# Kernel optimization log

Measured on AMD Instinct MI355X. Metric: run time of the kernel, lower is better.

The kernel has to match this reference:

```python
import jax, jax.numpy as jnp
import numpy as np

B, LQ, LK, D, H = 8, 512, 512, 512, 128

def setup_inputs() -> dict:
    key = jax.random.key(0)
    k1, k2, k3, k4, k5 = jax.random.split(key, 5)
    qs = jax.random.normal(k1, (B, LQ, D), dtype=jnp.float32)
    ks = jax.random.normal(k2, (B, LK, D), dtype=jnp.float32)
    # Dense kernels: flax Dense stores kernel as [in_features, out_features]
    Wq = jax.random.normal(k3, (D, H), dtype=jnp.float32) / np.sqrt(D)
    Wk = jax.random.normal(k4, (D, H), dtype=jnp.float32) / np.sqrt(D)
    wv = jax.random.normal(k5, (H,), dtype=jnp.float32) / np.sqrt(H)
    return {"qs": qs, "ks": ks, "Wq": Wq, "Wk": Wk, "wv": wv}

def reference(qs, ks, Wq, Wk, wv):
    # Project queries and keys into the shared hidden space: [B,Lq,H], [B,Lk,H]
    q = jnp.einsum("bqd,dh->bqh", qs, Wq)
    k = jnp.einsum("bkd,dh->bkh", ks, Wk)
    # Broadcast-add -> tanh -> linear reduce over H: scores [B,Lq,Lk]
    feats = jnp.tanh(q[:, :, None, :] + k[:, None, :, :])  # [B,Lq,Lk,H]
    return jnp.einsum("bqkh,h->bqk", feats, wv)
```

## Files before the change

### kernel.cpp

```cpp
#include <hip/hip_runtime.h>
#include <hip/hip_bf16.h>
#include <cstdint>

#define B_   8
#define LQ_  512
#define LK_  512
#define D_   512
#define H_   128

typedef __attribute__((ext_vector_type(8))) short  short8;
typedef __attribute__((ext_vector_type(4))) float  float4v;

#define TANH_C 2.8853900817779268f

__device__ __forceinline__ short bf16rne(float x) {
  uint32_t u = __float_as_uint(x);
  return (short)((u + 0x7fffu + ((u >> 16) & 1u)) >> 16);
}

__global__ __launch_bounds__(256) void prep_kernel(
    const float* __restrict__ Wq, const float* __restrict__ Wk,
    const float* __restrict__ wv,
    short* __restrict__ WqF, short* __restrict__ WkF,
    float* __restrict__ w2, float* __restrict__ W0buf) {
  int g = blockIdx.x * 256 + threadIdx.x;
  if (blockIdx.x == 0) {
    int t = threadIdx.x;
    if (t < H_) w2[t] = -2.0f * wv[t];
    if (t == H_) {
      float s = 0.f;
      for (int h = 0; h < H_; ++h) s += wv[h];
      W0buf[0] = s;
    }
  }
  int m = g >> 13;
  int r = g & 8191;
  int l  = r & 63;
  int kb = (r >> 6) & 15;
  int nt = r >> 10;
  int col = nt * 16 + (l & 15);
  int k0  = kb * 32 + ((l >> 4) << 3);
  const float* W = m ? Wk : Wq;
  short8 f;
#pragma unroll
  for (int j = 0; j < 8; ++j) f[j] = bf16rne(W[(k0 + j) * H_ + col]);
  ((short8*)(m ? WkF : WqF))[r] = f;
}

__global__ __launch_bounds__(256) void proj_kernel(
    const float* __restrict__ qs, const float* __restrict__ ks,
    const short* __restrict__ WqF, const short* __restrict__ WkF,
    float* __restrict__ qp, float* __restrict__ kp) {
  int blk  = blockIdx.x;
  int wave = threadIdx.x >> 6;
  int l    = threadIdx.x & 63;
  int grow = blk * 16;
  int m    = (grow >= 4096) ? 1 : 0;
  int r0   = grow - (m ? 4096 : 0);
  const float*  A  = m ? ks : qs;
  const short8* BF = (const short8*)(m ? WkF : WqF);
  float* out = m ? kp : qp;

  float4v acc[2];
  acc[0] = (float4v){0.f, 0.f, 0.f, 0.f};
  acc[1] = (float4v){0.f, 0.f, 0.f, 0.f};

  int quad = l >> 4;
  int arow = r0 + (l & 15);
  const float* aptr = A + (size_t)arow * D_ + quad * 8;
  int t0 = wave * 2;

#pragma unroll 4
  for (int kb = 0; kb < 16; ++kb) {
    float4v a0 = *(const float4v*)(aptr + kb * 32);
    float4v a1 = *(const float4v*)(aptr + kb * 32 + 4);
    short8 af;
#pragma unroll
    for (int j = 0; j < 4; ++j) { af[j] = bf16rne(a0[j]); af[j + 4] = bf16rne(a1[j]); }
#pragma unroll
    for (int tt = 0; tt < 2; ++tt) {
      short8 bf = BF[((t0 + tt) * 16 + kb) * 64 + l];
      acc[tt] = __builtin_amdgcn_mfma_f32_16x16x32_bf16(af, bf, acc[tt], 0, 0, 0);
    }
  }

#pragma unroll
  for (int tt = 0; tt < 2; ++tt)
#pragma unroll
    for (int r = 0; r < 4; ++r) {
      int row = r0 + quad * 4 + r;
      int col = (t0 + tt) * 16 + (l & 15);
      out[(size_t)row * H_ + col] = __builtin_amdgcn_exp2f(acc[tt][r] * TANH_C);
    }
}

__global__ __launch_bounds__(256) void score_kernel(
    const float* __restrict__ qp, const float* __restrict__ kp,
    const float* __restrict__ w2, const float* __restrict__ W0buf,
    float* __restrict__ out) {
  __shared__ float qt[32 * 68];
  __shared__ float kt[32 * 68];
  __shared__ float wl[H_];

  int b = blockIdx.z, qtile = blockIdx.y, ktile = blockIdx.x;
  int t = threadIdx.x;
  int tx = t & 15, ty = t >> 4;

  const float* qbase = qp + (size_t)(b * LQ_ + qtile * 32) * H_;
  const float* kbase = kp + (size_t)(b * LK_ + ktile * 32) * H_;

  float W0 = W0buf[0];

  if (t < 32) *(float4v*)&wl[t * 4] = *(const float4v*)&w2[t * 4];

  float accs[2][2];
  const float4v ones = (float4v){1.f, 1.f, 1.f, 1.f};
#pragma unroll
  for (int i = 0; i < 2; ++i)
#pragma unroll
    for (int j = 0; j < 2; ++j) accs[i][j] = 0.f;

  int lr = t >> 4, lc = t & 15;

  for (int hc = 0; hc < 2; ++hc) {
    __syncthreads();
#pragma unroll
    for (int s = 0; s < 2; ++s) {
      int row = lr + 16 * s;
      *(float4v*)&qt[row * 68 + lc * 4] =
          *(const float4v*)&qbase[row * H_ + hc * 64 + lc * 4];
      *(float4v*)&kt[row * 68 + lc * 4] =
          *(const float4v*)&kbase[row * H_ + hc * 64 + lc * 4];
    }
    __syncthreads();

#pragma unroll
    for (int h0 = 0; h0 < 64; h0 += 4) {
      float4v qv[2], kv[2];
#pragma unroll
      for (int i = 0; i < 2; ++i) qv[i] = *(const float4v*)&qt[(ty + 16 * i) * 68 + h0];
#pragma unroll
      for (int j = 0; j < 2; ++j) kv[j] = *(const float4v*)&kt[(tx + 16 * j) * 68 + h0];
      float4v w4 = *(const float4v*)&wl[hc * 64 + h0];

#pragma unroll
      for (int i = 0; i < 2; ++i)
#pragma unroll
        for (int j = 0; j < 2; ++j) {
          float4v den = __builtin_elementwise_fma(qv[i], kv[j], ones);
          float d01 = den[0] * den[1];
          float d23 = den[2] * den[3];
          float n01 = fmaf(w4[1], den[0], w4[0] * den[1]);
          float n23 = fmaf(w4[3], den[2], w4[2] * den[3]);
          float big = fmaf(n01, d23, n23 * d01);
          float r   = __builtin_amdgcn_rcpf(d01 * d23);
          accs[i][j] = fmaf(big, r, accs[i][j]);
        }
    }
  }

  size_t ob = (size_t)(b * LQ_ + qtile * 32) * LK_ + ktile * 32;
#pragma unroll
  for (int i = 0; i < 2; ++i)
#pragma unroll
    for (int j = 0; j < 2; ++j)
      out[ob + (size_t)(ty + 16 * i) * LK_ + tx + 16 * j] = W0 + accs[i][j];
}

extern "C" void kernel_launch(void* const* d_in, const int* in_sizes, int n_in,
                              void* d_out, int out_size, void* d_ws, size_t ws_size,
                              hipStream_t stream) {
  const float* qs = (const float*)d_in[0];
  const float* ks = (const float*)d_in[1];
  const float* Wq = (const float*)d_in[2];
  const float* Wk = (const float*)d_in[3];
  const float* wv = (const float*)d_in[4];
  float* out = (float*)d_out;

  char* ws = (char*)d_ws;
  short* WqF  = (short*)ws;
  short* WkF  = (short*)(ws + (128 << 10));
  float* qp   = (float*)(ws + (256 << 10));
  float* kp   = (float*)(ws + (256 << 10) + (2 << 20));
  float* w2   = (float*)(ws + (256 << 10) + (4 << 20));
  float* W0b  = (float*)(ws + (256 << 10) + (4 << 20) + 512);

  prep_kernel<<<64, 256, 0, stream>>>(Wq, Wk, wv, WqF, WkF, w2, W0b);
  proj_kernel<<<512, 256, 0, stream>>>(qs, ks, WqF, WkF, qp, kp);
  score_kernel<<<dim3(16, 16, 8), 256, 0, stream>>>(qp, kp, w2, W0b, out);
}
```

Before: 108.8 us.

## Enlarge score-kernel register tile to 4x4 and use per-element reciprocals

The score kernel now computes a 64x32 output tile with 128 threads, each holding a 4x4 block of outputs instead of 2x2. This raises the number of LDS operands reused per load and means fewer, larger blocks. The inner math drops the trick that combined four reciprocals into one shared rcp. It now takes four separate rcp instructions and accumulates into float4 vectors that are summed at the end. The extra transcendental instructions and the higher register pressure from 64 accumulators may offset the reuse gain.

```diff
diff --git a/kernel.cpp b/kernel.cpp
--- a/kernel.cpp
+++ b/kernel.cpp
@@ -94,77 +94,83 @@
     }
 }
 
-__global__ __launch_bounds__(256) void score_kernel(
+__global__ __launch_bounds__(128, 2) void score_kernel(
     const float* __restrict__ qp, const float* __restrict__ kp,
     const float* __restrict__ w2, const float* __restrict__ W0buf,
     float* __restrict__ out) {
-  __shared__ float qt[32 * 68];
+  __shared__ float qt[64 * 68];
   __shared__ float kt[32 * 68];
   __shared__ float wl[H_];
 
   int b = blockIdx.z, qtile = blockIdx.y, ktile = blockIdx.x;
   int t = threadIdx.x;
-  int tx = t & 15, ty = t >> 4;
+  int tx = t & 7, ty = t >> 3;
 
-  const float* qbase = qp + (size_t)(b * LQ_ + qtile * 32) * H_;
+  const float* qbase = qp + (size_t)(b * LQ_ + qtile * 64) * H_;
   const float* kbase = kp + (size_t)(b * LK_ + ktile * 32) * H_;
 
   float W0 = W0buf[0];
 
   if (t < 32) *(float4v*)&wl[t * 4] = *(const float4v*)&w2[t * 4];
 
-  float accs[2][2];
+  float4v acc4[4][4];
   const float4v ones = (float4v){1.f, 1.f, 1.f, 1.f};
 #pragma unroll
-  for (int i = 0; i < 2; ++i)
+  for (int i = 0; i < 4; ++i)
 #pragma unroll
-    for (int j = 0; j < 2; ++j) accs[i][j] = 0.f;
+    for (int j = 0; j < 4; ++j) acc4[i][j] = (float4v){0.f, 0.f, 0.f, 0.f};
 
   int lr = t >> 4, lc = t & 15;
 
   for (int hc = 0; hc < 2; ++hc) {
     __syncthreads();
 #pragma unroll
-    for (int s = 0; s < 2; ++s) {
-      int row = lr + 16 * s;
+    for (int s = 0; s < 8; ++s) {
+      int row = lr + 8 * s;
       *(float4v*)&qt[row * 68 + lc * 4] =
           *(const float4v*)&qbase[row * H_ + hc * 64 + lc * 4];
+    }
+#pragma unroll
+    for (int s = 0; s < 4; ++s) {
+      int row = lr + 8 * s;
       *(float4v*)&kt[row * 68 + lc * 4] =
           *(const float4v*)&kbase[row * H_ + hc * 64 + lc * 4];
     }
     __syncthreads();
 
+#pragma unroll 4
+    for (int h0 = 0; h0 < 64; h0 += 4) {
+      float4v qv[4], kv[4];
 #pragma unroll
-    for (int h0 = 0; h0 < 64; h0 += 4) {
-      float4v qv[2], kv[2];
+      for (int i = 0; i < 4; ++i) qv[i] = *(const float4v*)&qt[(ty + 16 * i) * 68 + h0];
 #pragma unroll
-      for (int i = 0; i < 2; ++i) qv[i] = *(const float4v*)&qt[(ty + 16 * i) * 68 + h0];
-#pragma unroll
-      for (int j = 0; j < 2; ++j) kv[j] = *(const float4v*)&kt[(tx + 16 * j) * 68 + h0];
+      for (int j = 0; j < 4; ++j) kv[j] = *(const float4v*)&kt[(tx + 8 * j) * 68 + h0];
       float4v w4 = *(const float4v*)&wl[hc * 64 + h0];
 
 #pragma unroll
-      for (int i = 0; i < 2; ++i)
+      for (int i = 0; i < 4; ++i)
 #pragma unroll
-        for (int j = 0; j < 2; ++j) {
+        for (int j = 0; j < 4; ++j) {
           float4v den = __builtin_elementwise_fma(qv[i], kv[j], ones);
-          float d01 = den[0] * den[1];
-          float d23 = den[2] * den[3];
-          float n01 = fmaf(w4[1], den[0], w4[0] * den[1]);
-          float n23 = fmaf(w4[3], den[2], w4[2] * den[3]);
-          float big = fmaf(n01, d23, n23 * d01);
-          float r   = __builtin_amdgcn_rcpf(d01 * d23);
-          accs[i][j] = fmaf(big, r, accs[i][j]);
+          float4v r;
+          r[0] = __builtin_amdgcn_rcpf(den[0]);
+          r[1] = __builtin_amdgcn_rcpf(den[1]);
+          r[2] = __builtin_amdgcn_rcpf(den[2]);
+          r[3] = __builtin_amdgcn_rcpf(den[3]);
+          acc4[i][j] = __builtin_elementwise_fma(w4, r, acc4[i][j]);
         }
     }
   }
 
-  size_t ob = (size_t)(b * LQ_ + qtile * 32) * LK_ + ktile * 32;
+  size_t ob = (size_t)(b * LQ_ + qtile * 64) * LK_ + ktile * 32;
 #pragma unroll
-  for (int i = 0; i < 2; ++i)
+  for (int i = 0; i < 4; ++i)
 #pragma unroll
-    for (int j = 0; j < 2; ++j)
-      out[ob + (size_t)(ty + 16 * i) * LK_ + tx + 16 * j] = W0 + accs[i][j];
+    for (int j = 0; j < 4; ++j) {
+      float4v a = acc4[i][j];
+      out[ob + (size_t)(ty + 16 * i) * LK_ + tx + 8 * j] =
+          W0 + ((a[0] + a[1]) + (a[2] + a[3]));
+    }
 }
 
 extern "C" void kernel_launch(void* const* d_in, const int* in_sizes, int n_in,
@@ -187,5 +193,5 @@
 
   prep_kernel<<<64, 256, 0, stream>>>(Wq, Wk, wv, WqF, WkF, w2, W0b);
   proj_kernel<<<512, 256, 0, stream>>>(qs, ks, WqF, WkF, qp, kp);
-  score_kernel<<<dim3(16, 16, 8), 256, 0, stream>>>(qp, kp, w2, W0b, out);
+  score_kernel<<<dim3(16, 8, 8), 128, 0, stream>>>(qp, kp, w2, W0b, out);
 }
```

Result: slower. 112.3 us (+3.1%).
